# Optimization experiments

Measured on AMD Instinct MI355X. Metric: run time of the kernel, lower is better.

The kernel has to match this reference:

```python
import jax, jax.numpy as jnp
import numpy as np

T, H, E, I, SI, TOP_K = 4096, 2048, 16, 1024, 4096, 1


def setup_inputs() -> dict:
    key = jax.random.key(0)
    ks = jax.random.split(key, 8)
    s_h = 1.0 / np.sqrt(H)
    s_i = 1.0 / np.sqrt(I)
    s_si = 1.0 / np.sqrt(SI)
    return {
        "hidden_states": jax.random.normal(ks[0], (T, H), jnp.float32),
        "router_w": jax.random.normal(ks[1], (E, H), jnp.float32) * s_h,
        "w_gate": jax.random.normal(ks[2], (E, H, I), jnp.float32) * s_h,
        "w_up": jax.random.normal(ks[3], (E, H, I), jnp.float32) * s_h,
        "w_down": jax.random.normal(ks[4], (E, I, H), jnp.float32) * s_i,
        "ws_gate": jax.random.normal(ks[5], (H, SI), jnp.float32) * s_h,
        "ws_up": jax.random.normal(ks[6], (H, SI), jnp.float32) * s_h,
        "ws_down": jax.random.normal(ks[7], (SI, H), jnp.float32) * s_si,
    }


def reference(hidden_states, router_w, w_gate, w_up, w_down, ws_gate, ws_up, ws_down):
    x = hidden_states  # [T, H]
    # Router: logits -> top-k -> sigmoid weights (Llama4RenormalizeMoeRoutingMethod)
    logits = jnp.einsum("th,eh->te", x, router_w)              # [T, E]
    top_vals, top_idx = jax.lax.top_k(logits, TOP_K)            # [T, K]
    weights = jax.nn.sigmoid(top_vals)                          # [T, K]
    # dispatch[t, e] = router weight if expert e selected for token t, else 0
    onehot = jax.nn.one_hot(top_idx, E, dtype=x.dtype)          # [T, K, E]
    dispatch = jnp.einsum("tke,tk->te", onehot, weights)        # [T, E]
    # Routed experts: router weight applied on input (commutes through the
    # linear gate/up projections as a per-(t,e) scalar applied before SiLU).
    g = jnp.einsum("th,ehi->tei", x, w_gate) * dispatch[:, :, None]  # [T, E, I]
    u = jnp.einsum("th,ehi->tei", x, w_up) * dispatch[:, :, None]    # [T, E, I]
    act = jax.nn.silu(g) * u                                          # [T, E, I]
    # Unselected experts contribute exactly 0 (act==0 there), so summing over
    # E in the down projection is the combine step.
    routed = jnp.einsum("tei,eih->th", act, w_down)             # [T, H]
    # Shared expert (SiLU-gated MLP on the unscaled hidden states)
    shared = (jax.nn.silu(x @ ws_gate) * (x @ ws_up)) @ ws_down  # [T, H]
    return shared + routed
```

## Files before the change

### kernel.cpp

```cpp
#include <hip/hip_runtime.h>
#include <hip/hip_bf16.h>

typedef unsigned short u16;
typedef unsigned int   u32;
typedef __attribute__((ext_vector_type(8))) short short8;
typedef __attribute__((ext_vector_type(4))) float f32x4;

#define T_TOK 4096
#define HDIM  2048
#define NEXP  16
#define IDIM  1024
#define SIDIM 4096
#define RCAP  6144
#define NTIL  48

#define O_WT      0u
#define O_EIDX    16384u
#define O_CNT     32768u
#define O_POS     32832u
#define O_PADOFF  32896u
#define O_TILEEXP 33024u
#define O_TOKROW  33280u
#define O_XBF     65536u
#define O_XSC     (O_XBF  + 2u*T_TOK*HDIM)
#define O_ACTS    (O_XSC  + 2u*RCAP*HDIM)
#define O_ACTR    (O_ACTS + 2u*T_TOK*SIDIM)
#define O_WSGT    (O_ACTR + 2u*RCAP*IDIM)
#define O_WSUT    (O_WSGT + 2u*SIDIM*HDIM)
#define O_WSDT    (O_WSUT + 2u*SIDIM*HDIM)
#define O_WGT     (O_WSDT + 2u*HDIM*SIDIM)
#define O_WUT     (O_WGT  + 2u*NEXP*IDIM*HDIM)
#define O_WDT     (O_WUT  + 2u*NEXP*IDIM*HDIM)

__device__ __forceinline__ u16 f2b(float f) {
  u32 u = __float_as_uint(f);
  u = (u + 0x7FFFu + ((u >> 16) & 1u)) >> 16;
  return (u16)u;
}

#define GLDS16(g, l) __builtin_amdgcn_global_load_lds( \
    (const __attribute__((address_space(1))) void*)(g), \
    (__attribute__((address_space(3))) void*)(l), 16, 0, 0)
#define BARX() __builtin_amdgcn_s_barrier()
#define SETPRIO(x) __builtin_amdgcn_s_setprio(x)
#define WAITVM(n) asm volatile("s_waitcnt vmcnt(" #n ")" ::: "memory")

__global__ __launch_bounds__(256) void router_k(
    const float* __restrict__ x, const float* __restrict__ rw,
    float* __restrict__ wt, int* __restrict__ eidx, int* __restrict__ cnt,
    u16* __restrict__ xbf) {
  int w = threadIdx.x >> 6, l = threadIdx.x & 63;
  int t = blockIdx.x * 4 + w;
  double acc[NEXP];
#pragma unroll
  for (int e = 0; e < NEXP; ++e) acc[e] = 0.0;
  const float* xp = x + (size_t)t * HDIM;
  u16* xo = xbf + (size_t)t * HDIM;
  for (int hb = 0; hb < HDIM; hb += 256) {
    float4 xv = *(const float4*)(xp + hb + l * 4);
    uint2 o;
    o.x = (u32)f2b(xv.x) | ((u32)f2b(xv.y) << 16);
    o.y = (u32)f2b(xv.z) | ((u32)f2b(xv.w) << 16);
    *(uint2*)(xo + hb + l * 4) = o;
#pragma unroll
    for (int e = 0; e < NEXP; ++e) {
      float4 wv = *(const float4*)(rw + (size_t)e * HDIM + hb + l * 4);
      acc[e] += (double)xv.x * wv.x + (double)xv.y * wv.y
              + (double)xv.z * wv.z + (double)xv.w * wv.w;
    }
  }
#pragma unroll
  for (int e = 0; e < NEXP; ++e) {
    double v = acc[e];
#pragma unroll
    for (int off = 32; off; off >>= 1) v += __shfl_xor(v, off, 64);
    acc[e] = v;
  }
  if (l == 0) {
    double best = acc[0]; int be = 0;
#pragma unroll
    for (int e = 1; e < NEXP; ++e) if (acc[e] > best) { best = acc[e]; be = e; }
    wt[t] = 1.0f / (1.0f + __expf(-(float)best));
    eidx[t] = be;
    atomicAdd(&cnt[be], 1);
  }
}

__global__ void scan_k(const int* __restrict__ cnt, int* __restrict__ pad_off,
                       int* __restrict__ tile_exp, int* __restrict__ pos,
                       int* __restrict__ tok_row) {
  if (threadIdx.x == 0) {
    for (int i = 0; i < 64; ++i) tile_exp[i] = -1;
    int run = 0;
    for (int e = 0; e < NEXP; ++e) {
      pad_off[e] = run;
      int pc = ((cnt[e] + 127) >> 7) << 7;
      for (int tt = run >> 7; tt < (run + pc) >> 7; ++tt) tile_exp[tt] = e;
      run += pc;
      pos[e] = 0;
    }
    pad_off[NEXP] = run;
  }
  for (int i = threadIdx.x; i < RCAP; i += 256) tok_row[i] = -1;
}

__global__ void assign_k(const int* __restrict__ eidx, const int* __restrict__ pad_off,
                         int* __restrict__ pos, int* __restrict__ tok_row) {
  int t = blockIdx.x * 256 + threadIdx.x;
  if (t >= T_TOK) return;
  int e = eidx[t];
  int r = atomicAdd(&pos[e], 1);
  tok_row[pad_off[e] + r] = t;
}

__global__ __launch_bounds__(256) void gather_k(
    const float* __restrict__ x, const float* __restrict__ wt,
    const int* __restrict__ tok_row, u16* __restrict__ xsc) {
  int g = blockIdx.x;
  int tid = threadIdx.x;
  u16* dst = xsc + (size_t)g * HDIM;
  int t = tok_row[g];
  if (t < 0) {
    uint2 z; z.x = 0u; z.y = 0u;
#pragma unroll
    for (int i = 0; i < 2; ++i) *(uint2*)(dst + i * 1024 + tid * 4) = z;
  } else {
    float s = wt[t];
    const float* src = x + (size_t)t * HDIM;
#pragma unroll
    for (int i = 0; i < 2; ++i) {
      int c = i * 1024 + tid * 4;
      float4 v = *(const float4*)(src + c);
      uint2 o;
      o.x = (u32)f2b(v.x * s) | ((u32)f2b(v.y * s) << 16);
      o.y = (u32)f2b(v.z * s) | ((u32)f2b(v.w * s) << 16);
      *(uint2*)(dst + c) = o;
    }
  }
}

__device__ __forceinline__ void conv_tile(
    const float* __restrict__ src, u16* __restrict__ dst, int K, int N,
    int bx, int ky, u32 (*lt)[36], int tid) {
  const int n0 = bx * 64, k0 = ky * 64;
  const int l = tid & 63, w = tid >> 6;
  const float* sp = src + (size_t)(k0 + w * 16) * N + n0 + l;
  u32 p[8];
#pragma unroll
  for (int i = 0; i < 8; ++i) {
    float a = sp[(size_t)(2 * i) * N];
    float b = sp[(size_t)(2 * i + 1) * N];
    p[i] = (u32)f2b(a) | ((u32)f2b(b) << 16);
  }
  *(uint4*)&lt[l][w * 8 + 0] = make_uint4(p[0], p[1], p[2], p[3]);
  *(uint4*)&lt[l][w * 8 + 4] = make_uint4(p[4], p[5], p[6], p[7]);
  __syncthreads();
  const int c = tid & 7, n2 = tid >> 3;
#pragma unroll
  for (int rnd = 0; rnd < 2; ++rnd) {
    int n = n2 + rnd * 32;
    uint4 v = *(const uint4*)&lt[n][c * 4];
    *(uint4*)(dst + (size_t)(n0 + n) * K + k0 + c * 8) = v;
  }
}

__global__ __launch_bounds__(256) void megaconv(
    const float* __restrict__ wsg, const float* __restrict__ wsu,
    const float* __restrict__ wsd, const float* __restrict__ wg,
    const float* __restrict__ wu, const float* __restrict__ wd,
    u16* wsgT, u16* wsuT, u16* wsdT, u16* wgT, u16* wuT, u16* wdT) {
  __shared__ u32 lt[64][36];
  int idx = blockIdx.x, tid = threadIdx.x;
  if (idx < 2048) {
    conv_tile(wsg, wsgT, 2048, 4096, idx & 63, idx >> 6, lt, tid);
  } else if (idx < 4096) { idx -= 2048;
    conv_tile(wsu, wsuT, 2048, 4096, idx & 63, idx >> 6, lt, tid);
  } else if (idx < 12288) { idx -= 4096;
    int e = idx >> 9, r = idx & 511;
    conv_tile(wg + (size_t)e * HDIM * IDIM, wgT + (size_t)e * IDIM * HDIM,
              2048, 1024, r & 15, r >> 4, lt, tid);
  } else if (idx < 20480) { idx -= 12288;
    int e = idx >> 9, r = idx & 511;
    conv_tile(wu + (size_t)e * HDIM * IDIM, wuT + (size_t)e * IDIM * HDIM,
              2048, 1024, r & 15, r >> 4, lt, tid);
  } else if (idx < 22528) { idx -= 20480;
    conv_tile(wsd, wsdT, 4096, 2048, idx & 31, idx >> 5, lt, tid);
  } else { idx -= 22528;
    int e = idx >> 9, r = idx & 511;
    conv_tile(wd + (size_t)e * IDIM * HDIM, wdT + (size_t)e * HDIM * IDIM,
              1024, 2048, r & 31, r >> 5, lt, tid);
  }
}


__global__ __launch_bounds__(512, 2) void gu_sh8(
    const u16* __restrict__ A, const u16* __restrict__ Bg, const u16* __restrict__ Bu,
    u16* __restrict__ act) {
  extern __shared__ u16 sm[];
  u16* As  = sm;
  u16* Bsm = sm + 32768;
  const int bid = blockIdx.x;
  const int xcd = bid & 7, bi = bid >> 3;
  const int bx = xcd * 4 + (bi & 3), by = bi >> 2;
  const int m0 = by * 256, c0 = bx * 128;
  const int tid = threadIdx.x, l = tid & 63, wid = tid >> 6;
  const int wm = wid >> 1, wn = wid & 1;

  const int cpos = tid & 3, rr = tid >> 2;
  const int gc = (cpos ^ ((rr >> 1) & 3)) * 8;
  const u16* aS0 = A + (size_t)(m0 + rr) * HDIM + gc;
  const u16* aS1 = A + (size_t)(m0 + 128 + rr) * HDIM + gc;
  const int mat = (rr >> 6) & 1;
  const u16* bbase = mat ? Bu : Bg;
  const u16* bS0 = bbase + (size_t)(c0 + (rr & 63)) * HDIM + gc;
  const u16* bS1 = bbase + (size_t)(c0 + 64 + (rr & 63)) * HDIM + gc;
  const int ld0 = tid * 8, ld1 = (512 + tid) * 8;

#define STA_G(bb, kh, koff) do { \
    GLDS16(aS0 + (koff) + (kh) * 32, As + ((bb) * 2 + (kh)) * 8192 + ld0); \
    GLDS16(aS1 + (koff) + (kh) * 32, As + ((bb) * 2 + (kh)) * 8192 + ld1); } while (0)
#define STB_G(bb, kh, koff) do { \
    GLDS16(bS0 + (koff) + (kh) * 32, Bsm + ((bb) * 2 + (kh)) * 8192 + ld0); \
    GLDS16(bS1 + (koff) + (kh) * 32, Bsm + ((bb) * 2 + (kh)) * 8192 + ld1); } while (0)

  const int fch = ((l >> 4) ^ ((l >> 1) & 3)) * 8;
  int aoff[4], boff[8];
#pragma unroll
  for (int mf = 0; mf < 4; ++mf) aoff[mf] = (wm * 64 + mf * 16 + (l & 15)) * 32 + fch;
#pragma unroll
  for (int i = 0; i < 8; ++i) {
    int v = wn * 128 + (i >> 2) * 64 + (i & 3) * 16 + (l & 15);
    boff[i] = v * 32 + fch;
  }
#define LDA_G(bb, kh) do { const u16* s_ = As + ((bb) * 2 + (kh)) * 8192; \
    af[0] = *(const short8*)(s_ + aoff[0]); af[1] = *(const short8*)(s_ + aoff[1]); \
    af[2] = *(const short8*)(s_ + aoff[2]); af[3] = *(const short8*)(s_ + aoff[3]); } while (0)
#define LDB_G(bb, kh, h, d) do { const u16* s_ = Bsm + ((bb) * 2 + (kh)) * 8192; \
    d[0] = *(const short8*)(s_ + boff[(h) * 4 + 0]); d[1] = *(const short8*)(s_ + boff[(h) * 4 + 1]); \
    d[2] = *(const short8*)(s_ + boff[(h) * 4 + 2]); d[3] = *(const short8*)(s_ + boff[(h) * 4 + 3]); } while (0)
#define MM32_G() do { SETPRIO(1); \
    _Pragma("unroll") for (int mf = 0; mf < 4; ++mf) { \
      _Pragma("unroll") for (int nf = 0; nf < 4; ++nf) \
        acc[mf][nf] = __builtin_amdgcn_mfma_f32_16x16x32_bf16(af[mf], bfrA[nf], acc[mf][nf], 0, 0, 0); \
      _Pragma("unroll") for (int nf = 0; nf < 4; ++nf) \
        acc[mf][4 + nf] = __builtin_amdgcn_mfma_f32_16x16x32_bf16(af[mf], bfrB[nf], acc[mf][4 + nf], 0, 0, 0); \
    } SETPRIO(0); } while (0)

  f32x4 acc[4][8];
#pragma unroll
  for (int i = 0; i < 4; ++i)
#pragma unroll
    for (int j = 0; j < 8; ++j)
#pragma unroll
      for (int r = 0; r < 4; ++r) acc[i][j][r] = 0.0f;
  short8 af[4], bfrA[4], bfrB[4];

  STA_G(0, 0, 0); STB_G(0, 0, 0); STA_G(0, 1, 0); STB_G(0, 1, 0);
  WAITVM(4); BARX();
  const int NT = HDIM / 64;
  for (int t = 0; t < NT - 1; ++t) {
    const int b = t & 1, nb = b ^ 1, kn = (t + 1) * 64;
    LDA_G(b, 0); LDB_G(b, 0, 0, bfrA); LDB_G(b, 0, 1, bfrB);
    STA_G(nb, 0, kn); STB_G(nb, 0, kn);
    BARX(); MM32_G(); WAITVM(4); BARX();
    LDA_G(b, 1); LDB_G(b, 1, 0, bfrA); LDB_G(b, 1, 1, bfrB);
    STA_G(nb, 1, kn); STB_G(nb, 1, kn);
    BARX(); MM32_G(); WAITVM(4); BARX();
  }
  { const int b = (NT - 1) & 1;
    LDA_G(b, 0); LDB_G(b, 0, 0, bfrA); LDB_G(b, 0, 1, bfrB);
    BARX(); MM32_G(); WAITVM(0); BARX();
    LDA_G(b, 1); LDB_G(b, 1, 0, bfrA); LDB_G(b, 1, 1, bfrB);
    MM32_G();
  }
#pragma unroll
  for (int mf = 0; mf < 4; ++mf)
#pragma unroll
    for (int nf = 0; nf < 4; ++nf) {
      int col = c0 + wn * 64 + nf * 16 + (l & 15);
      int rowb = m0 + wm * 64 + mf * 16 + (l >> 4) * 4;
#pragma unroll
      for (int r = 0; r < 4; ++r) {
        float g = acc[mf][nf][r], u = acc[mf][4 + nf][r];
        float s = g / (1.0f + __expf(-g));
        act[(size_t)(rowb + r) * SIDIM + col] = f2b(s * u);
      }
    }
#undef STA_G
#undef STB_G
#undef LDA_G
#undef LDB_G
#undef MM32_G
}

__global__ __launch_bounds__(512, 2) void dn_sh8(
    const u16* __restrict__ A, const u16* __restrict__ B, float* __restrict__ out) {
  extern __shared__ u16 sm[];
  u16* As  = sm;
  u16* Bsm = sm + 32768;
  const int bid = blockIdx.x;
  const int xcd = bid & 7, bi = bid >> 3;
  const int bx = xcd * 2 + (bi & 1), by = bi >> 1;
  const int m0 = by * 256, c0 = bx * 128;
  const int tid = threadIdx.x, l = tid & 63, wid = tid >> 6;
  const int wm = wid >> 1, wn = wid & 1;

  const int cpos = tid & 3, rr = tid >> 2;
  const int gc = (cpos ^ ((rr >> 1) & 3)) * 8;
  const u16* aS0 = A + (size_t)(m0 + rr) * SIDIM + gc;
  const u16* aS1 = A + (size_t)(m0 + 128 + rr) * SIDIM + gc;
  const u16* bS  = B + (size_t)(c0 + rr) * SIDIM + gc;
  const int ld0 = tid * 8, ld1 = (512 + tid) * 8;

#define STA_D(bb, kh, koff) do { \
    GLDS16(aS0 + (koff) + (kh) * 32, As + ((bb) * 2 + (kh)) * 8192 + ld0); \
    GLDS16(aS1 + (koff) + (kh) * 32, As + ((bb) * 2 + (kh)) * 8192 + ld1); } while (0)
#define STB_D(bb, kh, koff) \
    GLDS16(bS + (koff) + (kh) * 32, Bsm + ((bb) * 2 + (kh)) * 4096 + ld0)

  const int fch = ((l >> 4) ^ ((l >> 1) & 3)) * 8;
  int aoff[4], boff[4];
#pragma unroll
  for (int mf = 0; mf < 4; ++mf) aoff[mf] = (wm * 64 + mf * 16 + (l & 15)) * 32 + fch;
#pragma unroll
  for (int i = 0; i < 4; ++i) {
    int v = wn * 64 + (i >> 1) * 32 + (i & 1) * 16 + (l & 15);
    boff[i] = v * 32 + fch;
  }
#define LDA_D(bb, kh) do { const u16* s_ = As + ((bb) * 2 + (kh)) * 8192; \
    af[0] = *(const short8*)(s_ + aoff[0]); af[1] = *(const short8*)(s_ + aoff[1]); \
    af[2] = *(const short8*)(s_ + aoff[2]); af[3] = *(const short8*)(s_ + aoff[3]); } while (0)
#define LDB_D(bb, kh, h, d) do { const u16* s_ = Bsm + ((bb) * 2 + (kh)) * 4096; \
    d[0] = *(const short8*)(s_ + boff[(h) * 2 + 0]); \
    d[1] = *(const short8*)(s_ + boff[(h) * 2 + 1]); } while (0)
#define MM16_D() do { SETPRIO(1); \
    _Pragma("unroll") for (int mf = 0; mf < 4; ++mf) { \
      acc[mf][0] = __builtin_amdgcn_mfma_f32_16x16x32_bf16(af[mf], bfrA[0], acc[mf][0], 0, 0, 0); \
      acc[mf][1] = __builtin_amdgcn_mfma_f32_16x16x32_bf16(af[mf], bfrA[1], acc[mf][1], 0, 0, 0); \
      acc[mf][2] = __builtin_amdgcn_mfma_f32_16x16x32_bf16(af[mf], bfrB[0], acc[mf][2], 0, 0, 0); \
      acc[mf][3] = __builtin_amdgcn_mfma_f32_16x16x32_bf16(af[mf], bfrB[1], acc[mf][3], 0, 0, 0); \
    } SETPRIO(0); } while (0)

  f32x4 acc[4][4];
#pragma unroll
  for (int i = 0; i < 4; ++i)
#pragma unroll
    for (int j = 0; j < 4; ++j)
#pragma unroll
      for (int r = 0; r < 4; ++r) acc[i][j][r] = 0.0f;
  short8 af[4], bfrA[2], bfrB[2];

  STA_D(0, 0, 0); STB_D(0, 0, 0); STA_D(0, 1, 0); STB_D(0, 1, 0);
  WAITVM(3); BARX();
  const int NT = SIDIM / 64;
  for (int t = 0; t < NT - 1; ++t) {
    const int b = t & 1, nb = b ^ 1, kn = (t + 1) * 64;
    LDA_D(b, 0); LDB_D(b, 0, 0, bfrA); LDB_D(b, 0, 1, bfrB);
    STA_D(nb, 0, kn); STB_D(nb, 0, kn);
    BARX(); MM16_D(); WAITVM(3); BARX();
    LDA_D(b, 1); LDB_D(b, 1, 0, bfrA); LDB_D(b, 1, 1, bfrB);
    STA_D(nb, 1, kn); STB_D(nb, 1, kn);
    BARX(); MM16_D(); WAITVM(3); BARX();
  }
  { const int b = (NT - 1) & 1;
    LDA_D(b, 0); LDB_D(b, 0, 0, bfrA); LDB_D(b, 0, 1, bfrB);
    BARX(); MM16_D(); WAITVM(0); BARX();
    LDA_D(b, 1); LDB_D(b, 1, 0, bfrA); LDB_D(b, 1, 1, bfrB);
    MM16_D();
  }
#pragma unroll
  for (int mf = 0; mf < 4; ++mf)
#pragma unroll
    for (int nf = 0; nf < 4; ++nf) {
      int col = c0 + wn * 64 + (nf >> 1) * 32 + (nf & 1) * 16 + (l & 15);
      int rowb = m0 + wm * 64 + mf * 16 + (l >> 4) * 4;
#pragma unroll
      for (int r = 0; r < 4; ++r)
        out[(size_t)(rowb + r) * HDIM + col] = acc[mf][nf][r];
    }
#undef STA_D
#undef STB_D
#undef LDA_D
#undef LDB_D
#undef MM16_D
}

__global__ __launch_bounds__(256) void gu_r(
    const u16* __restrict__ A, const u16* __restrict__ BgT, const u16* __restrict__ BuT,
    u16* __restrict__ act, const int* __restrict__ tile_exp) {
  __shared__ __align__(16) u16 As[128 * 64];
  __shared__ __align__(16) u16 Bgs[64 * 64];
  __shared__ __align__(16) u16 Bus[64 * 64];
  const int tid = threadIdx.x;
  const int l = tid & 63, w = tid >> 6;
  const int wm = w >> 1, wn = w & 1;
  const int m0 = blockIdx.y * 128, n0 = blockIdx.x * 64;
  int e = tile_exp[blockIdx.y];
  if (e < 0) return;
  size_t eo = (size_t)e * IDIM * HDIM;
  const u16* Bg = BgT + eo + (size_t)n0 * HDIM;
  const u16* Bu = BuT + eo + (size_t)n0 * HDIM;
  f32x4 accg[4][2], accu[4][2];
#pragma unroll
  for (int i = 0; i < 4; ++i)
#pragma unroll
    for (int j = 0; j < 2; ++j)
#pragma unroll
      for (int r = 0; r < 4; ++r) { accg[i][j][r] = 0.0f; accu[i][j][r] = 0.0f; }
  const u16* Ab = A + (size_t)m0 * HDIM;

  for (int k0 = 0; k0 < HDIM; k0 += 64) {
    __syncthreads();
#pragma unroll
    for (int j = 0; j < 4; ++j) {
      int c = j * 256 + tid, r = c >> 3, cc = c & 7;
      GLDS16(Ab + (size_t)r * HDIM + k0 + ((cc ^ (r & 7)) * 8), &As[c * 8]);
    }
#pragma unroll
    for (int j = 0; j < 2; ++j) {
      int c = j * 256 + tid, r = c >> 3, cc = c & 7;
      int sc = (cc ^ (r & 7)) * 8;
      GLDS16(Bg + (size_t)r * HDIM + k0 + sc, &Bgs[c * 8]);
      GLDS16(Bu + (size_t)r * HDIM + k0 + sc, &Bus[c * 8]);
    }
    __syncthreads();
#pragma unroll
    for (int kh = 0; kh < 2; ++kh) {
      const int q = kh * 4 + (l >> 4);
      short8 af[4];
#pragma unroll
      for (int mf = 0; mf < 4; ++mf) {
        int r = wm * 64 + mf * 16 + (l & 15);
        af[mf] = *(const short8*)&As[r * 64 + ((q ^ (r & 7)) * 8)];
      }
      short8 bgf[2], buf2[2];
#pragma unroll
      for (int nf = 0; nf < 2; ++nf) {
        int n = wn * 32 + nf * 16 + (l & 15);
        bgf[nf]  = *(const short8*)&Bgs[n * 64 + ((q ^ (n & 7)) * 8)];
        buf2[nf] = *(const short8*)&Bus[n * 64 + ((q ^ (n & 7)) * 8)];
      }
#pragma unroll
      for (int mf = 0; mf < 4; ++mf)
#pragma unroll
        for (int nf = 0; nf < 2; ++nf) {
          accg[mf][nf] = __builtin_amdgcn_mfma_f32_16x16x32_bf16(af[mf], bgf[nf],  accg[mf][nf], 0, 0, 0);
          accu[mf][nf] = __builtin_amdgcn_mfma_f32_16x16x32_bf16(af[mf], buf2[nf], accu[mf][nf], 0, 0, 0);
        }
    }
  }
#pragma unroll
  for (int mf = 0; mf < 4; ++mf)
#pragma unroll
    for (int nf = 0; nf < 2; ++nf) {
      int col = n0 + wn * 32 + nf * 16 + (l & 15);
#pragma unroll
      for (int r = 0; r < 4; ++r) {
        int row = m0 + wm * 64 + mf * 16 + (l >> 4) * 4 + r;
        float g = accg[mf][nf][r], u = accu[mf][nf][r];
        float s = g / (1.0f + __expf(-g));
        act[(size_t)row * IDIM + col] = f2b(s * u);
      }
    }
}

__global__ __launch_bounds__(256) void dn_r(
    const u16* __restrict__ A, const u16* __restrict__ BT, float* __restrict__ out,
    const int* __restrict__ tile_exp, const int* __restrict__ tok_row) {
  __shared__ __align__(16) u16 As[128 * 64];
  __shared__ __align__(16) u16 Bs[128 * 64];
  const int tid = threadIdx.x;
  const int l = tid & 63, w = tid >> 6;
  const int wm = w >> 1, wn = w & 1;
  const int m0 = blockIdx.y * 128, n0 = blockIdx.x * 128;
  int e = tile_exp[blockIdx.y];
  if (e < 0) return;
  const u16* B = BT + (size_t)e * HDIM * IDIM + (size_t)n0 * IDIM;
  f32x4 acc[4][4];
#pragma unroll
  for (int i = 0; i < 4; ++i)
#pragma unroll
    for (int j = 0; j < 4; ++j)
#pragma unroll
      for (int r = 0; r < 4; ++r) acc[i][j][r] = 0.0f;
  const u16* Ab = A + (size_t)m0 * IDIM;

  for (int k0 = 0; k0 < IDIM; k0 += 64) {
    __syncthreads();
#pragma unroll
    for (int j = 0; j < 4; ++j) {
      int c = j * 256 + tid, r = c >> 3, cc = c & 7;
      GLDS16(Ab + (size_t)r * IDIM + k0 + ((cc ^ (r & 7)) * 8), &As[c * 8]);
    }
#pragma unroll
    for (int j = 0; j < 4; ++j) {
      int c = j * 256 + tid, r = c >> 3, cc = c & 7;
      GLDS16(B + (size_t)r * IDIM + k0 + ((cc ^ (r & 7)) * 8), &Bs[c * 8]);
    }
    __syncthreads();
#pragma unroll
    for (int kh = 0; kh < 2; ++kh) {
      const int q = kh * 4 + (l >> 4);
      short8 af[4];
#pragma unroll
      for (int mf = 0; mf < 4; ++mf) {
        int r = wm * 64 + mf * 16 + (l & 15);
        af[mf] = *(const short8*)&As[r * 64 + ((q ^ (r & 7)) * 8)];
      }
      short8 bf[4];
#pragma unroll
      for (int nf = 0; nf < 4; ++nf) {
        int n = wn * 64 + nf * 16 + (l & 15);
        bf[nf] = *(const short8*)&Bs[n * 64 + ((q ^ (n & 7)) * 8)];
      }
#pragma unroll
      for (int mf = 0; mf < 4; ++mf)
#pragma unroll
        for (int nf = 0; nf < 4; ++nf)
          acc[mf][nf] = __builtin_amdgcn_mfma_f32_16x16x32_bf16(af[mf], bf[nf], acc[mf][nf], 0, 0, 0);
    }
  }
#pragma unroll
  for (int mf = 0; mf < 4; ++mf)
#pragma unroll
    for (int nf = 0; nf < 4; ++nf) {
      int col = n0 + wn * 64 + nf * 16 + (l & 15);
#pragma unroll
      for (int r = 0; r < 4; ++r) {
        int grow = m0 + wm * 64 + mf * 16 + (l >> 4) * 4 + r;
        int t = tok_row[grow];
        if (t >= 0) out[(size_t)t * HDIM + col] += acc[mf][nf][r];
      }
    }
}

extern "C" void kernel_launch(void* const* d_in, const int* in_sizes, int n_in,
                              void* d_out, int out_size, void* d_ws, size_t ws_size,
                              hipStream_t stream) {
  const float* x   = (const float*)d_in[0];
  const float* rw  = (const float*)d_in[1];
  const float* wg  = (const float*)d_in[2];
  const float* wu  = (const float*)d_in[3];
  const float* wd  = (const float*)d_in[4];
  const float* wsg = (const float*)d_in[5];
  const float* wsu = (const float*)d_in[6];
  const float* wsd = (const float*)d_in[7];
  float* out = (float*)d_out;
  char* ws = (char*)d_ws;

  float* wt     = (float*)(ws + O_WT);
  int* eidx     = (int*)(ws + O_EIDX);
  int* cnt      = (int*)(ws + O_CNT);
  int* pos      = (int*)(ws + O_POS);
  int* pad_off  = (int*)(ws + O_PADOFF);
  int* tile_exp = (int*)(ws + O_TILEEXP);
  int* tok_row  = (int*)(ws + O_TOKROW);
  u16* xbf      = (u16*)(ws + O_XBF);
  u16* xsc      = (u16*)(ws + O_XSC);
  u16* acts     = (u16*)(ws + O_ACTS);
  u16* actr     = (u16*)(ws + O_ACTR);
  u16* wsgT     = (u16*)(ws + O_WSGT);
  u16* wsuT     = (u16*)(ws + O_WSUT);
  u16* wsdT     = (u16*)(ws + O_WSDT);
  u16* wgT      = (u16*)(ws + O_WGT);
  u16* wuT      = (u16*)(ws + O_WUT);
  u16* wdT      = (u16*)(ws + O_WDT);

  hipFuncSetAttribute((const void*)gu_sh8, hipFuncAttributeMaxDynamicSharedMemorySize, 131072);
  hipFuncSetAttribute((const void*)dn_sh8, hipFuncAttributeMaxDynamicSharedMemorySize, 98304);

  hipMemsetAsync(ws + O_CNT, 0, 128, stream);
  router_k<<<T_TOK / 4, 256, 0, stream>>>(x, rw, wt, eidx, cnt, xbf);
  scan_k<<<1, 256, 0, stream>>>(cnt, pad_off, tile_exp, pos, tok_row);
  assign_k<<<T_TOK / 256, 256, 0, stream>>>(eidx, pad_off, pos, tok_row);
  gather_k<<<RCAP, 256, 0, stream>>>(x, wt, tok_row, xsc);
  megaconv<<<30720, 256, 0, stream>>>(wsg, wsu, wsd, wg, wu, wd,
                                      wsgT, wsuT, wsdT, wgT, wuT, wdT);

  gu_sh8<<<512, 512, 131072, stream>>>(xbf, wsgT, wsuT, acts);
  gu_r<<<dim3(IDIM / 64, NTIL), 256, 0, stream>>>(xsc, wgT, wuT, actr, tile_exp);
  dn_sh8<<<256, 512, 98304, stream>>>(acts, wsdT, out);
  dn_r<<<dim3(HDIM / 128, NTIL), 256, 0, stream>>>(actr, wdT, out, tile_exp, tok_row);
}
```

Baseline: 667.7 us.

## Read fp32 expert weights directly in routed GEMMs, dropping per-call bf16 conversion

```diff
diff --git a/kernel.cpp b/kernel.cpp
--- a/kernel.cpp
+++ b/kernel.cpp
@@ -28,9 +28,6 @@
 #define O_WSGT    (O_ACTR + 2u*RCAP*IDIM)
 #define O_WSUT    (O_WSGT + 2u*SIDIM*HDIM)
 #define O_WSDT    (O_WSUT + 2u*SIDIM*HDIM)
-#define O_WGT     (O_WSDT + 2u*HDIM*SIDIM)
-#define O_WUT     (O_WGT  + 2u*NEXP*IDIM*HDIM)
-#define O_WDT     (O_WUT  + 2u*NEXP*IDIM*HDIM)
 
 __device__ __forceinline__ u16 f2b(float f) {
   u32 u = __float_as_uint(f);
@@ -166,29 +163,15 @@
 
 __global__ __launch_bounds__(256) void megaconv(
     const float* __restrict__ wsg, const float* __restrict__ wsu,
-    const float* __restrict__ wsd, const float* __restrict__ wg,
-    const float* __restrict__ wu, const float* __restrict__ wd,
-    u16* wsgT, u16* wsuT, u16* wsdT, u16* wgT, u16* wuT, u16* wdT) {
+    const float* __restrict__ wsd, u16* wsgT, u16* wsuT, u16* wsdT) {
   __shared__ u32 lt[64][36];
   int idx = blockIdx.x, tid = threadIdx.x;
   if (idx < 2048) {
     conv_tile(wsg, wsgT, 2048, 4096, idx & 63, idx >> 6, lt, tid);
   } else if (idx < 4096) { idx -= 2048;
     conv_tile(wsu, wsuT, 2048, 4096, idx & 63, idx >> 6, lt, tid);
-  } else if (idx < 12288) { idx -= 4096;
-    int e = idx >> 9, r = idx & 511;
-    conv_tile(wg + (size_t)e * HDIM * IDIM, wgT + (size_t)e * IDIM * HDIM,
-              2048, 1024, r & 15, r >> 4, lt, tid);
-  } else if (idx < 20480) { idx -= 12288;
-    int e = idx >> 9, r = idx & 511;
-    conv_tile(wu + (size_t)e * HDIM * IDIM, wuT + (size_t)e * IDIM * HDIM,
-              2048, 1024, r & 15, r >> 4, lt, tid);
-  } else if (idx < 22528) { idx -= 20480;
+  } else { idx -= 4096;
     conv_tile(wsd, wsdT, 4096, 2048, idx & 31, idx >> 5, lt, tid);
-  } else { idx -= 22528;
-    int e = idx >> 9, r = idx & 511;
-    conv_tile(wd + (size_t)e * IDIM * HDIM, wdT + (size_t)e * HDIM * IDIM,
-              1024, 2048, r & 31, r >> 5, lt, tid);
   }
 }
 
@@ -385,21 +368,22 @@
 #undef MM16_D
 }
 
-__global__ __launch_bounds__(256) void gu_r(
-    const u16* __restrict__ A, const u16* __restrict__ BgT, const u16* __restrict__ BuT,
+
+__global__ __launch_bounds__(256) void gu_rf(
+    const u16* __restrict__ A, const float* __restrict__ Bg0, const float* __restrict__ Bu0,
     u16* __restrict__ act, const int* __restrict__ tile_exp) {
   __shared__ __align__(16) u16 As[128 * 64];
-  __shared__ __align__(16) u16 Bgs[64 * 64];
-  __shared__ __align__(16) u16 Bus[64 * 64];
+  __shared__ __align__(16) u16 Bgs[64 * 72];
+  __shared__ __align__(16) u16 Bus[64 * 72];
   const int tid = threadIdx.x;
   const int l = tid & 63, w = tid >> 6;
   const int wm = w >> 1, wn = w & 1;
   const int m0 = blockIdx.y * 128, n0 = blockIdx.x * 64;
   int e = tile_exp[blockIdx.y];
   if (e < 0) return;
-  size_t eo = (size_t)e * IDIM * HDIM;
-  const u16* Bg = BgT + eo + (size_t)n0 * HDIM;
-  const u16* Bu = BuT + eo + (size_t)n0 * HDIM;
+  size_t eo = (size_t)e * HDIM * IDIM;
+  const float* Bg = Bg0 + eo;
+  const float* Bu = Bu0 + eo;
   f32x4 accg[4][2], accu[4][2];
 #pragma unroll
   for (int i = 0; i < 4; ++i)
@@ -416,12 +400,26 @@
       int c = j * 256 + tid, r = c >> 3, cc = c & 7;
       GLDS16(Ab + (size_t)r * HDIM + k0 + ((cc ^ (r & 7)) * 8), &As[c * 8]);
     }
-#pragma unroll
-    for (int j = 0; j < 2; ++j) {
-      int c = j * 256 + tid, r = c >> 3, cc = c & 7;
-      int sc = (cc ^ (r & 7)) * 8;
-      GLDS16(Bg + (size_t)r * HDIM + k0 + sc, &Bgs[c * 8]);
-      GLDS16(Bu + (size_t)r * HDIM + k0 + sc, &Bus[c * 8]);
+    {
+      const float* bp = Bg + (size_t)(k0 + w * 16) * IDIM + n0 + l;
+      u16 h[16];
+#pragma unroll
+      for (int i = 0; i < 16; ++i) h[i] = f2b(bp[(size_t)i * IDIM]);
+#pragma unroll
+      for (int j = 0; j < 4; ++j) {
+        uint2 v; v.x = (u32)h[4*j] | ((u32)h[4*j+1] << 16);
+        v.y = (u32)h[4*j+2] | ((u32)h[4*j+3] << 16);
+        *(uint2*)&Bgs[l * 72 + w * 16 + j * 4] = v;
+      }
+      bp = Bu + (size_t)(k0 + w * 16) * IDIM + n0 + l;
+#pragma unroll
+      for (int i = 0; i < 16; ++i) h[i] = f2b(bp[(size_t)i * IDIM]);
+#pragma unroll
+      for (int j = 0; j < 4; ++j) {
+        uint2 v; v.x = (u32)h[4*j] | ((u32)h[4*j+1] << 16);
+        v.y = (u32)h[4*j+2] | ((u32)h[4*j+3] << 16);
+        *(uint2*)&Bus[l * 72 + w * 16 + j * 4] = v;
+      }
     }
     __syncthreads();
 #pragma unroll
@@ -437,8 +435,8 @@
 #pragma unroll
       for (int nf = 0; nf < 2; ++nf) {
         int n = wn * 32 + nf * 16 + (l & 15);
-        bgf[nf]  = *(const short8*)&Bgs[n * 64 + ((q ^ (n & 7)) * 8)];
-        buf2[nf] = *(const short8*)&Bus[n * 64 + ((q ^ (n & 7)) * 8)];
+        bgf[nf]  = *(const short8*)&Bgs[n * 72 + q * 8];
+        buf2[nf] = *(const short8*)&Bus[n * 72 + q * 8];
       }
 #pragma unroll
       for (int mf = 0; mf < 4; ++mf)
@@ -464,23 +462,23 @@
     }
 }
 
-__global__ __launch_bounds__(256) void dn_r(
-    const u16* __restrict__ A, const u16* __restrict__ BT, float* __restrict__ out,
+__global__ __launch_bounds__(256) void dn_rf(
+    const u16* __restrict__ A, const float* __restrict__ B0, float* __restrict__ out,
     const int* __restrict__ tile_exp, const int* __restrict__ tok_row) {
   __shared__ __align__(16) u16 As[128 * 64];
-  __shared__ __align__(16) u16 Bs[128 * 64];
+  __shared__ __align__(16) u16 Bs[64 * 72];
   const int tid = threadIdx.x;
   const int l = tid & 63, w = tid >> 6;
   const int wm = w >> 1, wn = w & 1;
-  const int m0 = blockIdx.y * 128, n0 = blockIdx.x * 128;
+  const int m0 = blockIdx.y * 128, n0 = blockIdx.x * 64;
   int e = tile_exp[blockIdx.y];
   if (e < 0) return;
-  const u16* B = BT + (size_t)e * HDIM * IDIM + (size_t)n0 * IDIM;
-  f32x4 acc[4][4];
+  const float* B = B0 + (size_t)e * IDIM * HDIM;
+  f32x4 acc[4][2];
 #pragma unroll
   for (int i = 0; i < 4; ++i)
 #pragma unroll
-    for (int j = 0; j < 4; ++j)
+    for (int j = 0; j < 2; ++j)
 #pragma unroll
       for (int r = 0; r < 4; ++r) acc[i][j][r] = 0.0f;
   const u16* Ab = A + (size_t)m0 * IDIM;
@@ -492,10 +490,17 @@
       int c = j * 256 + tid, r = c >> 3, cc = c & 7;
       GLDS16(Ab + (size_t)r * IDIM + k0 + ((cc ^ (r & 7)) * 8), &As[c * 8]);
     }
-#pragma unroll
-    for (int j = 0; j < 4; ++j) {
-      int c = j * 256 + tid, r = c >> 3, cc = c & 7;
-      GLDS16(B + (size_t)r * IDIM + k0 + ((cc ^ (r & 7)) * 8), &Bs[c * 8]);
+    {
+      const float* bp = B + (size_t)(k0 + w * 16) * HDIM + n0 + l;
+      u16 h[16];
+#pragma unroll
+      for (int i = 0; i < 16; ++i) h[i] = f2b(bp[(size_t)i * HDIM]);
+#pragma unroll
+      for (int j = 0; j < 4; ++j) {
+        uint2 v; v.x = (u32)h[4*j] | ((u32)h[4*j+1] << 16);
+        v.y = (u32)h[4*j+2] | ((u32)h[4*j+3] << 16);
+        *(uint2*)&Bs[l * 72 + w * 16 + j * 4] = v;
+      }
     }
     __syncthreads();
 #pragma unroll
@@ -507,24 +512,24 @@
         int r = wm * 64 + mf * 16 + (l & 15);
         af[mf] = *(const short8*)&As[r * 64 + ((q ^ (r & 7)) * 8)];
       }
-      short8 bf[4];
-#pragma unroll
-      for (int nf = 0; nf < 4; ++nf) {
-        int n = wn * 64 + nf * 16 + (l & 15);
-        bf[nf] = *(const short8*)&Bs[n * 64 + ((q ^ (n & 7)) * 8)];
+      short8 bf[2];
+#pragma unroll
+      for (int nf = 0; nf < 2; ++nf) {
+        int n = wn * 32 + nf * 16 + (l & 15);
+        bf[nf] = *(const short8*)&Bs[n * 72 + q * 8];
       }
 #pragma unroll
       for (int mf = 0; mf < 4; ++mf)
 #pragma unroll
-        for (int nf = 0; nf < 4; ++nf)
+        for (int nf = 0; nf < 2; ++nf)
           acc[mf][nf] = __builtin_amdgcn_mfma_f32_16x16x32_bf16(af[mf], bf[nf], acc[mf][nf], 0, 0, 0);
     }
   }
 #pragma unroll
   for (int mf = 0; mf < 4; ++mf)
 #pragma unroll
-    for (int nf = 0; nf < 4; ++nf) {
-      int col = n0 + wn * 64 + nf * 16 + (l & 15);
+    for (int nf = 0; nf < 2; ++nf) {
+      int col = n0 + wn * 32 + nf * 16 + (l & 15);
 #pragma unroll
       for (int r = 0; r < 4; ++r) {
         int grow = m0 + wm * 64 + mf * 16 + (l >> 4) * 4 + r;
@@ -562,23 +567,19 @@
   u16* wsgT     = (u16*)(ws + O_WSGT);
   u16* wsuT     = (u16*)(ws + O_WSUT);
   u16* wsdT     = (u16*)(ws + O_WSDT);
-  u16* wgT      = (u16*)(ws + O_WGT);
-  u16* wuT      = (u16*)(ws + O_WUT);
-  u16* wdT      = (u16*)(ws + O_WDT);
 
   hipFuncSetAttribute((const void*)gu_sh8, hipFuncAttributeMaxDynamicSharedMemorySize, 131072);
   hipFuncSetAttribute((const void*)dn_sh8, hipFuncAttributeMaxDynamicSharedMemorySize, 98304);
 
   hipMemsetAsync(ws + O_CNT, 0, 128, stream);
+  megaconv<<<6144, 256, 0, stream>>>(wsg, wsu, wsd, wsgT, wsuT, wsdT);
   router_k<<<T_TOK / 4, 256, 0, stream>>>(x, rw, wt, eidx, cnt, xbf);
   scan_k<<<1, 256, 0, stream>>>(cnt, pad_off, tile_exp, pos, tok_row);
   assign_k<<<T_TOK / 256, 256, 0, stream>>>(eidx, pad_off, pos, tok_row);
   gather_k<<<RCAP, 256, 0, stream>>>(x, wt, tok_row, xsc);
-  megaconv<<<30720, 256, 0, stream>>>(wsg, wsu, wsd, wg, wu, wd,
-                                      wsgT, wsuT, wsdT, wgT, wuT, wdT);
 
   gu_sh8<<<512, 512, 131072, stream>>>(xbf, wsgT, wsuT, acts);
-  gu_r<<<dim3(IDIM / 64, NTIL), 256, 0, stream>>>(xsc, wgT, wuT, actr, tile_exp);
+  gu_rf<<<dim3(IDIM / 64, NTIL), 256, 0, stream>>>(xsc, wg, wu, actr, tile_exp);
   dn_sh8<<<256, 512, 98304, stream>>>(acts, wsdT, out);
-  dn_r<<<dim3(HDIM / 128, NTIL), 256, 0, stream>>>(actr, wdT, out, tile_exp, tok_row);
-}
+  dn_rf<<<dim3(HDIM / 64, NTIL), 256, 0, stream>>>(actr, wd, out, tile_exp, tok_row);
+}
```

Measured after the change: 569.2 us. -14.8%, faster.
